# Kernel optimization log

Hardware: AMD Instinct MI355X
Metric: run time of the kernel (lower is better)

## Reference

```python
import jax, jax.numpy as jnp
import numpy as np

B, C, H, W = 4, 256, 64, 64
C8 = C // 8

def setup_inputs() -> dict:
    key = jax.random.key(0)
    ks = jax.random.split(key, 7)
    s = 0.05
    return {
        "x": jax.random.normal(ks[0], (B, C, H, W), dtype=jnp.float32),
        "wq": jax.random.normal(ks[1], (C8, C), dtype=jnp.float32) * s,
        "bq": jax.random.normal(ks[2], (C8,), dtype=jnp.float32) * s,
        "wk": jax.random.normal(ks[3], (C8, C), dtype=jnp.float32) * s,
        "bk": jax.random.normal(ks[4], (C8,), dtype=jnp.float32) * s,
        "wv": jax.random.normal(ks[5], (C, C), dtype=jnp.float32) * s,
        "bv": jax.random.normal(ks[6], (C,), dtype=jnp.float32) * s,
    }

def reference(x, wq, bq, wk, bk, wv, bv):
    b, c, h, w = x.shape
    n = h * w
    xf = x.reshape(b, c, n)                                   # [B,C,N]
    q = jnp.einsum('oc,bcn->bon', wq, xf) + bq[:, None]       # [B,C/8,N]
    k = jnp.einsum('oc,bcn->bon', wk, xf) + bk[:, None]       # [B,C/8,N]
    v = jnp.einsum('oc,bcn->bon', wv, xf) + bv[:, None]       # [B,C,N]
    # attention[b, i, j] = softmax_j( q[b,:,i] . k[b,:,j] )  (no scaling, per original)
    scores = jnp.einsum('bon,bom->bnm', q, k)                 # [B,N,N]
    attn = jax.nn.softmax(scores, axis=-1)
    # out[b,c,i] = sum_j v[b,c,j] * attn[b,i,j]
    out = jnp.einsum('bcm,bnm->bcn', v, attn)                 # [B,C,N]
    return out.reshape(b, c, h, w) + x
```

## Files before the change

### kernel.cpp

```cpp
#include <hip/hip_runtime.h>
#include <cstdint>
#include <cstddef>

#define BB 4
#define CC 256
#define NN 4096
#define CO 32

typedef __attribute__((ext_vector_type(8))) short bf8;
typedef __attribute__((ext_vector_type(4))) float f4;
typedef __attribute__((ext_vector_type(2))) unsigned int u32x2;

#define AS1 __attribute__((address_space(1)))
#define AS3 __attribute__((address_space(3)))

__device__ __forceinline__ unsigned short f2bf(float f) {
    union { float f; unsigned int u; } c; c.f = f;
    unsigned int r = c.u + 0x7FFFu + ((c.u >> 16) & 1u);
    return (unsigned short)(r >> 16);
}
__device__ __forceinline__ float bf2f(unsigned short b) {
    union { unsigned int u; float f; } c; c.u = ((unsigned int)b) << 16;
    return c.f;
}
__device__ __forceinline__ unsigned int cvt_pk_bf16(float a, float b) {
    unsigned int r;
    asm("v_cvt_pk_bf16_f32 %0, %1, %2" : "=v"(r) : "v"(a), "v"(b));
    return r;
}

#define LDS_BARRIER()                                          \
    do {                                                       \
        __builtin_amdgcn_sched_barrier(0);                     \
        asm volatile("s_waitcnt lgkmcnt(0)" ::: "memory");     \
        __builtin_amdgcn_s_barrier();                          \
        __builtin_amdgcn_sched_barrier(0);                     \
    } while (0)

__global__ __launch_bounds__(512, 2) void k_prep(
        const float* __restrict__ x,
        const float* __restrict__ wq, const float* __restrict__ bq,
        const float* __restrict__ wk, const float* __restrict__ bk,
        const float* __restrict__ wv, const float* __restrict__ bv,
        unsigned short* __restrict__ q_hi, unsigned short* __restrict__ q_lo,
        unsigned short* __restrict__ k_hi, unsigned short* __restrict__ k_lo,
        unsigned short* __restrict__ vws) {
    __shared__ float xT[64 * 256];
    int blk = blockIdx.x;
    int it = blk & 63, b = blk >> 6;
    int i0 = it * 64;
    int tid = threadIdx.x, w = tid >> 6, lane = tid & 63;
    int lr = lane & 15, lg = lane >> 4;

    {
        const float* xp = x + (size_t)b * CC * NN + i0;
        int cl = tid >> 4;
        int il = (tid & 15) * 4;
#pragma unroll
        for (int pass = 0; pass < 8; ++pass) {
            int c = pass * 32 + cl;
            f4 v = *(const f4*)(xp + (size_t)c * NN + il);
#pragma unroll
            for (int jj = 0; jj < 4; ++jj) {
                int i = il + jj;
                xT[i * 256 + (((c >> 2) ^ (i & 7)) << 2) + (c & 3)] = v[jj];
            }
        }
    }
    __syncthreads();

    if (w < 4) {
        f4 acc[4] = {};
        for (int ks = 0; ks < 8; ++ks) {
            int i = w * 16 + lr;
            int kc = ks * 32 + lg * 8;
            f4 xa = *(const f4*)&xT[i * 256 + (((kc >> 2) ^ (i & 7)) << 2)];
            f4 xb = *(const f4*)&xT[i * 256 + ((((kc >> 2) + 1) ^ (i & 7)) << 2)];
            bf8 ahi, alo;
#pragma unroll
            for (int e = 0; e < 8; ++e) {
                float f = (e < 4) ? xa[e] : xb[e - 4];
                unsigned short hh = f2bf(f);
                ahi[e] = (short)hh;
                alo[e] = (short)f2bf(f - bf2f(hh));
            }
#pragma unroll
            for (int u = 0; u < 4; ++u) {
                int o = u * 16 + lr;
                const float* wrow = (u < 2) ? (wq + (size_t)o * CC)
                                            : (wk + (size_t)(o - 32) * CC);
                bf8 bhi, blo;
#pragma unroll
                for (int e = 0; e < 8; ++e) {
                    float wvv = wrow[ks * 32 + lg * 8 + e];
                    unsigned short hh = f2bf(wvv);
                    bhi[e] = (short)hh;
                    blo[e] = (short)f2bf(wvv - bf2f(hh));
                }
                acc[u] = __builtin_amdgcn_mfma_f32_16x16x32_bf16(alo, bhi, acc[u], 0, 0, 0);
                acc[u] = __builtin_amdgcn_mfma_f32_16x16x32_bf16(ahi, blo, acc[u], 0, 0, 0);
                acc[u] = __builtin_amdgcn_mfma_f32_16x16x32_bf16(ahi, bhi, acc[u], 0, 0, 0);
            }
        }
#pragma unroll
        for (int u = 0; u < 4; ++u) {
            int o = u * 16 + lr;
            float bias = (u < 2) ? bq[o] : bk[o - 32];
#pragma unroll
            for (int r = 0; r < 4; ++r) {
                int i = i0 + w * 16 + lg * 4 + r;
                float v = acc[u][r] + bias;
                unsigned short hh = f2bf(v);
                unsigned short ll = f2bf(v - bf2f(hh));
                if (u < 2) {
                    size_t off = ((size_t)b * NN + i) * CO + o;
                    q_hi[off] = hh; q_lo[off] = ll;
                } else {
                    size_t off = ((size_t)b * NN + i) * CO + (o - 32);
                    k_hi[off] = hh; k_lo[off] = ll;
                }
            }
        }
    } else {
        int cb = (w - 4) * 64;
        f4 acc[4][4];
#pragma unroll
        for (int u = 0; u < 4; ++u) {
            f4 bias4;
#pragma unroll
            for (int r = 0; r < 4; ++r) bias4[r] = bv[cb + u * 16 + lg * 4 + r];
#pragma unroll
            for (int t = 0; t < 4; ++t) acc[u][t] = bias4;
        }
        for (int ks = 0; ks < 8; ++ks) {
            bf8 bfr[4];
#pragma unroll
            for (int t = 0; t < 4; ++t) {
                int i = t * 16 + lr;
                int kc = ks * 32 + lg * 8;
                f4 xa = *(const f4*)&xT[i * 256 + (((kc >> 2) ^ (i & 7)) << 2)];
                f4 xb = *(const f4*)&xT[i * 256 + ((((kc >> 2) + 1) ^ (i & 7)) << 2)];
#pragma unroll
                for (int e = 0; e < 8; ++e)
                    bfr[t][e] = (short)f2bf((e < 4) ? xa[e] : xb[e - 4]);
            }
#pragma unroll
            for (int u = 0; u < 4; ++u) {
                const float* wrow = wv + (size_t)(cb + u * 16 + lr) * CC + ks * 32 + lg * 8;
                bf8 afr;
#pragma unroll
                for (int e = 0; e < 8; ++e) afr[e] = (short)f2bf(wrow[e]);
#pragma unroll
                for (int t = 0; t < 4; ++t)
                    acc[u][t] = __builtin_amdgcn_mfma_f32_16x16x32_bf16(afr, bfr[t], acc[u][t], 0, 0, 0);
            }
        }
#pragma unroll
        for (int u = 0; u < 4; ++u)
#pragma unroll
            for (int t = 0; t < 4; ++t)
#pragma unroll
                for (int r = 0; r < 4; ++r) {
                    int c = cb + u * 16 + lg * 4 + r;
                    vws[((size_t)b * CC + c) * NN + i0 + t * 16 + lr] = f2bf(acc[u][t][r]);
                }
    }
}

__global__ __launch_bounds__(512, 4) void k_attn(
        const unsigned short* __restrict__ q_hi, const unsigned short* __restrict__ q_lo,
        const unsigned short* __restrict__ k_hi, const unsigned short* __restrict__ k_lo,
        const unsigned short* __restrict__ vws,
        const float* __restrict__ x, float* __restrict__ out) {
    __shared__ unsigned short Vt[2][8192];
    __shared__ unsigned short K2[2][4096];
    __shared__ unsigned short Pt[4096];
    __shared__ float lsum_s[2][64];

    int m = blockIdx.x;
    int xcd = m & 7;
    int b = xcd >> 1;
    int t128 = ((m >> 3) << 1) + (xcd & 1);
    int qblk = t128 >> 1;
    int hc = t128 & 1;
    int i0 = qblk * 64;
    int cb0 = hc * 128;
    int tid = threadIdx.x, w = tid >> 6, lane = tid & 63;
    int lr = lane & 15, lg = lane >> 4;
    int a = w & 3, h = w >> 2;
    int lr7 = lr & 7;

    bf8 qfh, qfl;
    {
        size_t off = ((size_t)b * NN + i0 + a * 16 + lr) * CO + lg * 8;
        qfh = *(const bf8*)(q_hi + off);
        qfl = *(const bf8*)(q_lo + off);
    }

    const unsigned short* vrow  = vws  + (size_t)b * CC * NN;
    const unsigned short* khrow = k_hi + (size_t)b * NN * CO;
    const unsigned short* klrow = k_lo + (size_t)b * NN * CO;

    int l3 = lane >> 3, sl = lane & 7;
    int us = sl ^ l3;
    const unsigned short* vsrc = vrow + (size_t)(cb0 + w * 16 + l3) * NN + us * 8;
    const unsigned short* kbp = (us < 4) ? (khrow + us * 8) : (klrow + (us - 4) * 8);
    const unsigned short* ksrc = kbp + (size_t)(w * 8 + l3) * CO;

    auto stage = [&](int jt, int p) {
        int j0 = jt * 64;
#pragma unroll
        for (int n = 0; n < 2; ++n) {
            __builtin_amdgcn_global_load_lds(
                (const AS1 void*)(vsrc + (size_t)(n * 8) * NN + j0),
                (AS3 void*)(&Vt[p][(w * 16 + n * 8) * 64]), 16, 0, 0);
        }
        __builtin_amdgcn_global_load_lds(
            (const AS1 void*)(ksrc + (size_t)j0 * CO),
            (AS3 void*)(&K2[p][(w * 8) * 64]), 16, 0, 0);
    };

    f4 acc[4] = {};
    float lsum = 0.f;

    stage(0, 0);
    __syncthreads();

    for (int jt = 0; jt < 64; ++jt) {
        int p = jt & 1;
        if (jt < 63) stage(jt + 1, p ^ 1);
#pragma unroll
        for (int jj = 0; jj < 2; ++jj) {
            int jl = h * 32 + jj * 16 + lr;
            bf8 kfh = *(const bf8*)&K2[p][jl * 64 + ((lg ^ lr7)) * 8];
            bf8 kfl = *(const bf8*)&K2[p][jl * 64 + (((4 | lg) ^ lr7)) * 8];
            f4 s = {};
            s = __builtin_amdgcn_mfma_f32_16x16x32_bf16(kfh, qfl, s, 0, 0, 0);
            s = __builtin_amdgcn_mfma_f32_16x16x32_bf16(kfl, qfh, s, 0, 0, 0);
            s = __builtin_amdgcn_mfma_f32_16x16x32_bf16(kfh, qfh, s, 0, 0, 0);
            float e0 = __expf(s[0]), e1 = __expf(s[1]), e2 = __expf(s[2]), e3 = __expf(s[3]);
            lsum += (e0 + e1) + (e2 + e3);
            u32x2 d;
            d[0] = cvt_pk_bf16(e0, e1);
            d[1] = cvt_pk_bf16(e2, e3);
            int slot = (h * 4 + jj * 2 + (lg >> 1)) ^ lr7;
            *(u32x2*)&Pt[(a * 16 + lr) * 64 + slot * 8 + (lg & 1) * 4] = d;
        }
        LDS_BARRIER();
        __builtin_amdgcn_s_setprio(1);
#pragma unroll
        for (int ks = 0; ks < 2; ++ks) {
            bf8 pb[4], vf;
#pragma unroll
            for (int qt = 0; qt < 4; ++qt)
                pb[qt] = *(const bf8*)&Pt[(qt * 16 + lr) * 64 + (((ks * 4 + lg) ^ lr7)) * 8];
            vf = *(const bf8*)&Vt[p][(w * 16 + lr) * 64 + (((ks * 4 + lg) ^ lr7)) * 8];
#pragma unroll
            for (int qt = 0; qt < 4; ++qt)
                acc[qt] = __builtin_amdgcn_mfma_f32_16x16x32_bf16(vf, pb[qt], acc[qt], 0, 0, 0);
        }
        __builtin_amdgcn_s_setprio(0);
        __syncthreads();
    }

    lsum += __shfl_xor(lsum, 16, 64);
    lsum += __shfl_xor(lsum, 32, 64);
    if (lane < 16) lsum_s[h][a * 16 + lane] = lsum;
    __syncthreads();

#pragma unroll
    for (int qt = 0; qt < 4; ++qt) {
        float li = 1.0f / (lsum_s[0][qt * 16 + lr] + lsum_s[1][qt * 16 + lr]);
        int iq = i0 + qt * 16 + lr;
#pragma unroll
        for (int r = 0; r < 4; ++r) {
            int c = cb0 + w * 16 + lg * 4 + r;
            size_t off = ((size_t)(b * CC + c)) * NN + iq;
            out[off] = acc[qt][r] * li + x[off];
        }
    }
}

extern "C" void kernel_launch(void* const* d_in, const int* in_sizes, int n_in,
                              void* d_out, int out_size, void* d_ws, size_t ws_size,
                              hipStream_t stream) {
    const float* x  = (const float*)d_in[0];
    const float* wq = (const float*)d_in[1];
    const float* bq = (const float*)d_in[2];
    const float* wk = (const float*)d_in[3];
    const float* bk = (const float*)d_in[4];
    const float* wv = (const float*)d_in[5];
    const float* bv = (const float*)d_in[6];
    float* out = (float*)d_out;
    char* ws = (char*)d_ws;
    unsigned short* qh = (unsigned short*)(ws);
    unsigned short* ql = (unsigned short*)(ws + 1048576);
    unsigned short* kh = (unsigned short*)(ws + 2097152);
    unsigned short* kl = (unsigned short*)(ws + 3145728);
    unsigned short* vv = (unsigned short*)(ws + 4194304);

    hipLaunchKernelGGL(k_prep, dim3(256), dim3(512), 0, stream,
                       x, wq, bq, wk, bk, wv, bv, qh, ql, kh, kl, vv);
    hipLaunchKernelGGL(k_attn, dim3(512), dim3(512), 0, stream,
                       qh, ql, kh, kl, vv, x, out);
}
```

Baseline: 98.33 us.

## Switch attention to 32x32 MFMA, triple-buffer K and double-buffer P

Rewrites the attention kernel's inner loop to use 32x32x16 bf16 MFMAs for both QK^T and PV. Only half of the waves compute scores. K now uses a 3-stage LDS ring and P a double buffer, so the loop drops to one barrier per iteration with a partial vmcnt wait, letting loads overlap compute. The aim is fewer instructions and less synchronisation per tile. The trade-off is idle waves during the score phase, more LDS use, and new swizzle patterns that have to stay conflict-free and correct.

```diff
diff --git a/kernel.cpp b/kernel.cpp
--- a/kernel.cpp
+++ b/kernel.cpp
@@ -9,6 +9,7 @@
 
 typedef __attribute__((ext_vector_type(8))) short bf8;
 typedef __attribute__((ext_vector_type(4))) float f4;
+typedef __attribute__((ext_vector_type(16))) float f16f;
 typedef __attribute__((ext_vector_type(2))) unsigned int u32x2;
 
 #define AS1 __attribute__((address_space(1)))
@@ -28,14 +29,6 @@
     asm("v_cvt_pk_bf16_f32 %0, %1, %2" : "=v"(r) : "v"(a), "v"(b));
     return r;
 }
-
-#define LDS_BARRIER()                                          \
-    do {                                                       \
-        __builtin_amdgcn_sched_barrier(0);                     \
-        asm volatile("s_waitcnt lgkmcnt(0)" ::: "memory");     \
-        __builtin_amdgcn_s_barrier();                          \
-        __builtin_amdgcn_sched_barrier(0);                     \
-    } while (0)
 
 __global__ __launch_bounds__(512, 2) void k_prep(
         const float* __restrict__ x,
@@ -172,10 +165,10 @@
         const unsigned short* __restrict__ k_hi, const unsigned short* __restrict__ k_lo,
         const unsigned short* __restrict__ vws,
         const float* __restrict__ x, float* __restrict__ out) {
-    __shared__ unsigned short Vt[2][8192];
-    __shared__ unsigned short K2[2][4096];
-    __shared__ unsigned short Pt[4096];
-    __shared__ float lsum_s[2][64];
+    __shared__ __align__(16) unsigned short Vt[2][8192];
+    __shared__ __align__(16) unsigned short K2[3][4096];
+    __shared__ __align__(16) unsigned short P2[2][2][2048];
+    __shared__ float lsum_s[2][2][32];
 
     int m = blockIdx.x;
     int xcd = m & 7;
@@ -186,98 +179,109 @@
     int i0 = qblk * 64;
     int cb0 = hc * 128;
     int tid = threadIdx.x, w = tid >> 6, lane = tid & 63;
-    int lr = lane & 15, lg = lane >> 4;
-    int a = w & 3, h = w >> 2;
-    int lr7 = lr & 7;
-
-    bf8 qfh, qfl;
-    {
-        size_t off = ((size_t)b * NN + i0 + a * 16 + lr) * CO + lg * 8;
-        qfh = *(const bf8*)(q_hi + off);
-        qfl = *(const bf8*)(q_lo + off);
-    }
-
-    const unsigned short* vrow  = vws  + (size_t)b * CC * NN;
-    const unsigned short* khrow = k_hi + (size_t)b * NN * CO;
-    const unsigned short* klrow = k_lo + (size_t)b * NN * CO;
-
+    int l31 = lane & 31, h = lane >> 5;
+    int fsw = (lane & 7) ^ ((lane >> 3) & 3);
+    int jh = w & 1, qh = w >> 1;
+    int cs = w & 3, qhp = w >> 2;
+
+    bf8 qfh[2], qfl[2];
+    if (w < 4) {
+        size_t qoff = ((size_t)b * NN + i0 + qh * 32 + l31) * CO + h * 8;
+        qfh[0] = *(const bf8*)(q_hi + qoff);
+        qfl[0] = *(const bf8*)(q_lo + qoff);
+        qfh[1] = *(const bf8*)(q_hi + qoff + 16);
+        qfl[1] = *(const bf8*)(q_lo + qoff + 16);
+    }
+
+    const unsigned short* vrow = vws + (size_t)b * CC * NN;
     int l3 = lane >> 3, sl = lane & 7;
-    int us = sl ^ l3;
-    const unsigned short* vsrc = vrow + (size_t)(cb0 + w * 16 + l3) * NN + us * 8;
-    const unsigned short* kbp = (us < 4) ? (khrow + us * 8) : (klrow + (us - 4) * 8);
-    const unsigned short* ksrc = kbp + (size_t)(w * 8 + l3) * CO;
-
-    auto stage = [&](int jt, int p) {
-        int j0 = jt * 64;
-#pragma unroll
-        for (int n = 0; n < 2; ++n) {
-            __builtin_amdgcn_global_load_lds(
-                (const AS1 void*)(vsrc + (size_t)(n * 8) * NN + j0),
-                (AS3 void*)(&Vt[p][(w * 16 + n * 8) * 64]), 16, 0, 0);
-        }
-        __builtin_amdgcn_global_load_lds(
-            (const AS1 void*)(ksrc + (size_t)j0 * CO),
+    int usV0 = sl ^ l3 ^ ((2 * w) & 3);
+    int usV1 = usV0 ^ 1;
+    const unsigned short* vsrc0 = vrow + (size_t)(cb0 + w * 16 + l3) * NN + usV0 * 8;
+    const unsigned short* vsrc1 = vrow + (size_t)(cb0 + w * 16 + 8 + l3) * NN + usV1 * 8;
+    int usK = sl ^ l3 ^ (w & 3);
+    const unsigned short* kbase = (usK < 4) ? (k_hi + (size_t)b * NN * CO + usK * 8)
+                                            : (k_lo + (size_t)b * NN * CO + (usK - 4) * 8);
+    const unsigned short* ksrc = kbase + (size_t)(w * 8 + l3) * CO;
+
+    auto stageV = [&](int jt, int p) {
+        int j0 = ((jt < 64) ? jt : 63) * 64;
+        __builtin_amdgcn_global_load_lds((const AS1 void*)(vsrc0 + j0),
+            (AS3 void*)(&Vt[p][(w * 16) * 64]), 16, 0, 0);
+        __builtin_amdgcn_global_load_lds((const AS1 void*)(vsrc1 + j0),
+            (AS3 void*)(&Vt[p][(w * 16 + 8) * 64]), 16, 0, 0);
+    };
+    auto stageK = [&](int jt, int p) {
+        int j0 = ((jt < 64) ? jt : 63) * 64;
+        __builtin_amdgcn_global_load_lds((const AS1 void*)(ksrc + (size_t)j0 * CO),
             (AS3 void*)(&K2[p][(w * 8) * 64]), 16, 0, 0);
     };
 
-    f4 acc[4] = {};
+    f16f acc = {};
     float lsum = 0.f;
 
-    stage(0, 0);
+    stageV(0, 0); stageK(0, 0); stageK(1, 1);
     __syncthreads();
 
     for (int jt = 0; jt < 64; ++jt) {
-        int p = jt & 1;
-        if (jt < 63) stage(jt + 1, p ^ 1);
-#pragma unroll
-        for (int jj = 0; jj < 2; ++jj) {
-            int jl = h * 32 + jj * 16 + lr;
-            bf8 kfh = *(const bf8*)&K2[p][jl * 64 + ((lg ^ lr7)) * 8];
-            bf8 kfl = *(const bf8*)&K2[p][jl * 64 + (((4 | lg) ^ lr7)) * 8];
-            f4 s = {};
-            s = __builtin_amdgcn_mfma_f32_16x16x32_bf16(kfh, qfl, s, 0, 0, 0);
-            s = __builtin_amdgcn_mfma_f32_16x16x32_bf16(kfl, qfh, s, 0, 0, 0);
-            s = __builtin_amdgcn_mfma_f32_16x16x32_bf16(kfh, qfh, s, 0, 0, 0);
-            float e0 = __expf(s[0]), e1 = __expf(s[1]), e2 = __expf(s[2]), e3 = __expf(s[3]);
-            lsum += (e0 + e1) + (e2 + e3);
-            u32x2 d;
-            d[0] = cvt_pk_bf16(e0, e1);
-            d[1] = cvt_pk_bf16(e2, e3);
-            int slot = (h * 4 + jj * 2 + (lg >> 1)) ^ lr7;
-            *(u32x2*)&Pt[(a * 16 + lr) * 64 + slot * 8 + (lg & 1) * 4] = d;
-        }
-        LDS_BARRIER();
+        int pv = jt & 1;
+        int pk = jt % 3;
+        if (w < 4) {
+            const unsigned short* Kp = &K2[pk][(jh * 32 + l31) * 64];
+            f16f s = {};
+#pragma unroll
+            for (int dc = 0; dc < 2; ++dc) {
+                bf8 kfh = *(const bf8*)(Kp + (((2 * dc + h) ^ fsw) * 8));
+                bf8 kfl = *(const bf8*)(Kp + (((4 + 2 * dc + h) ^ fsw) * 8));
+                s = __builtin_amdgcn_mfma_f32_32x32x16_bf16(kfh, qfl[dc], s, 0, 0, 0);
+                s = __builtin_amdgcn_mfma_f32_32x32x16_bf16(kfl, qfh[dc], s, 0, 0, 0);
+                s = __builtin_amdgcn_mfma_f32_32x32x16_bf16(kfh, qfh[dc], s, 0, 0, 0);
+            }
+            unsigned int pk32[8];
+#pragma unroll
+            for (int i = 0; i < 8; ++i) {
+                float e0 = __expf(s[2 * i]), e1 = __expf(s[2 * i + 1]);
+                lsum += e0 + e1;
+                pk32[i] = cvt_pk_bf16(e0, e1);
+            }
+            unsigned short* Pp = &P2[pv][qh][l31 * 64 + h * 4];
+#pragma unroll
+            for (int g = 0; g < 4; ++g) {
+                u32x2 d2; d2[0] = pk32[2 * g]; d2[1] = pk32[2 * g + 1];
+                *(u32x2*)(Pp + (((jh * 4 + g) ^ fsw) * 8)) = d2;
+            }
+        }
+        stageK(jt + 2, (jt + 2) % 3);
+        __builtin_amdgcn_sched_barrier(0);
+        asm volatile("s_waitcnt vmcnt(1) lgkmcnt(0)" ::: "memory");
+        __builtin_amdgcn_s_barrier();
+        __builtin_amdgcn_sched_barrier(0);
         __builtin_amdgcn_s_setprio(1);
-#pragma unroll
-        for (int ks = 0; ks < 2; ++ks) {
-            bf8 pb[4], vf;
-#pragma unroll
-            for (int qt = 0; qt < 4; ++qt)
-                pb[qt] = *(const bf8*)&Pt[(qt * 16 + lr) * 64 + (((ks * 4 + lg) ^ lr7)) * 8];
-            vf = *(const bf8*)&Vt[p][(w * 16 + lr) * 64 + (((ks * 4 + lg) ^ lr7)) * 8];
-#pragma unroll
-            for (int qt = 0; qt < 4; ++qt)
-                acc[qt] = __builtin_amdgcn_mfma_f32_16x16x32_bf16(vf, pb[qt], acc[qt], 0, 0, 0);
+        {
+            const unsigned short* Pr = &P2[pv][qhp][l31 * 64];
+            const unsigned short* Vr = &Vt[pv][(cs * 32 + l31) * 64];
+#pragma unroll
+            for (int kc = 0; kc < 4; ++kc) {
+                bf8 pb = *(const bf8*)(Pr + (((2 * kc + h) ^ fsw) * 8));
+                bf8 vf = *(const bf8*)(Vr + (((2 * kc + h) ^ fsw) * 8));
+                acc = __builtin_amdgcn_mfma_f32_32x32x16_bf16(vf, pb, acc, 0, 0, 0);
+            }
         }
         __builtin_amdgcn_s_setprio(0);
-        __syncthreads();
-    }
-
-    lsum += __shfl_xor(lsum, 16, 64);
+        stageV(jt + 1, pv ^ 1);
+    }
+
     lsum += __shfl_xor(lsum, 32, 64);
-    if (lane < 16) lsum_s[h][a * 16 + lane] = lsum;
+    if (w < 4 && lane < 32) lsum_s[qh][jh][l31] = lsum;
     __syncthreads();
 
-#pragma unroll
-    for (int qt = 0; qt < 4; ++qt) {
-        float li = 1.0f / (lsum_s[0][qt * 16 + lr] + lsum_s[1][qt * 16 + lr]);
-        int iq = i0 + qt * 16 + lr;
-#pragma unroll
-        for (int r = 0; r < 4; ++r) {
-            int c = cb0 + w * 16 + lg * 4 + r;
-            size_t off = ((size_t)(b * CC + c)) * NN + iq;
-            out[off] = acc[qt][r] * li + x[off];
-        }
+    float linv = 1.0f / (lsum_s[qhp][0][l31] + lsum_s[qhp][1][l31]);
+    int iq = i0 + qhp * 32 + l31;
+#pragma unroll
+    for (int r = 0; r < 16; ++r) {
+        int c = cb0 + cs * 32 + (r & 3) + 8 * (r >> 2) + 4 * h;
+        size_t off = ((size_t)(b * CC + c)) * NN + iq;
+        out[off] = acc[r] * linv + x[off];
     }
 }
 
```

Result: slower. 103.1 us (+4.9%).

## Load V directly to registers and switch PV to 32x32x16 MFMA

Applied to the files above, without the earlier changes.

The P·V stage now uses 32x32x16 bf16 MFMAs, with each wave owning a 32-channel by 32-query tile. V fragments are loaded straight from global memory into double-buffered registers one tile ahead, so the V staging buffer in LDS is removed. A manual vmcnt wait plus barrier replaces __syncthreads, and the P tile uses a new row-dependent swizzle. The aim is to cut LDS traffic and footprint and to issue fewer, larger MFMAs. In exchange it adds register pressure and relies on global load latency being hidden within one iteration.

```diff
diff --git a/kernel.cpp b/kernel.cpp
--- a/kernel.cpp
+++ b/kernel.cpp
@@ -9,6 +9,7 @@
 
 typedef __attribute__((ext_vector_type(8))) short bf8;
 typedef __attribute__((ext_vector_type(4))) float f4;
+typedef __attribute__((ext_vector_type(16))) float f16f;
 typedef __attribute__((ext_vector_type(2))) unsigned int u32x2;
 
 #define AS1 __attribute__((address_space(1)))
@@ -172,9 +173,8 @@
         const unsigned short* __restrict__ k_hi, const unsigned short* __restrict__ k_lo,
         const unsigned short* __restrict__ vws,
         const float* __restrict__ x, float* __restrict__ out) {
-    __shared__ unsigned short Vt[2][8192];
-    __shared__ unsigned short K2[2][4096];
-    __shared__ unsigned short Pt[4096];
+    __shared__ __align__(16) unsigned short K2[2][4096];
+    __shared__ __align__(16) unsigned short Pt[4096];
     __shared__ float lsum_s[2][64];
 
     int m = blockIdx.x;
@@ -186,9 +186,10 @@
     int i0 = qblk * 64;
     int cb0 = hc * 128;
     int tid = threadIdx.x, w = tid >> 6, lane = tid & 63;
-    int lr = lane & 15, lg = lane >> 4;
+    int lr = lane & 15, lg = lane >> 4, lr7 = lr & 7;
     int a = w & 3, h = w >> 2;
-    int lr7 = lr & 7;
+    int l31 = lane & 31, hh = lane >> 5;
+    int cs = w & 3, qhp = w >> 2;
 
     bf8 qfh, qfl;
     {
@@ -197,43 +198,37 @@
         qfl = *(const bf8*)(q_lo + off);
     }
 
-    const unsigned short* vrow  = vws  + (size_t)b * CC * NN;
-    const unsigned short* khrow = k_hi + (size_t)b * NN * CO;
-    const unsigned short* klrow = k_lo + (size_t)b * NN * CO;
-
     int l3 = lane >> 3, sl = lane & 7;
-    int us = sl ^ l3;
-    const unsigned short* vsrc = vrow + (size_t)(cb0 + w * 16 + l3) * NN + us * 8;
-    const unsigned short* kbp = (us < 4) ? (khrow + us * 8) : (klrow + (us - 4) * 8);
-    const unsigned short* ksrc = kbp + (size_t)(w * 8 + l3) * CO;
-
-    auto stage = [&](int jt, int p) {
-        int j0 = jt * 64;
-#pragma unroll
-        for (int n = 0; n < 2; ++n) {
-            __builtin_amdgcn_global_load_lds(
-                (const AS1 void*)(vsrc + (size_t)(n * 8) * NN + j0),
-                (AS3 void*)(&Vt[p][(w * 16 + n * 8) * 64]), 16, 0, 0);
-        }
-        __builtin_amdgcn_global_load_lds(
-            (const AS1 void*)(ksrc + (size_t)j0 * CO),
+    int usK = sl ^ l3;
+    const unsigned short* kbase = (usK < 4) ? (k_hi + (size_t)b * NN * CO + usK * 8)
+                                            : (k_lo + (size_t)b * NN * CO + (usK - 4) * 8);
+    const unsigned short* ksrc = kbase + (size_t)(w * 8 + l3) * CO;
+    auto stageK = [&](int jt, int p) {
+        int j0 = ((jt < 64) ? jt : 63) * 64;
+        __builtin_amdgcn_global_load_lds((const AS1 void*)(ksrc + (size_t)j0 * CO),
             (AS3 void*)(&K2[p][(w * 8) * 64]), 16, 0, 0);
     };
 
-    f4 acc[4] = {};
+    const unsigned short* vsrcb = vws + ((size_t)b * CC + cb0 + cs * 32 + l31) * NN + hh * 8;
+
+    f16f acc = {};
     float lsum = 0.f;
-
-    stage(0, 0);
+    bf8 vA[4], vB[4];
+
+    stageK(0, 0);
+#pragma unroll
+    for (int kc = 0; kc < 4; ++kc) vA[kc] = *(const bf8*)(vsrcb + kc * 16);
     __syncthreads();
 
-    for (int jt = 0; jt < 64; ++jt) {
+    auto iter = [&](int jt, bf8 (&vc)[4], bf8 (&vn)[4]) {
         int p = jt & 1;
-        if (jt < 63) stage(jt + 1, p ^ 1);
-#pragma unroll
-        for (int jj = 0; jj < 2; ++jj) {
-            int jl = h * 32 + jj * 16 + lr;
-            bf8 kfh = *(const bf8*)&K2[p][jl * 64 + ((lg ^ lr7)) * 8];
-            bf8 kfl = *(const bf8*)&K2[p][jl * 64 + (((4 | lg) ^ lr7)) * 8];
+        stageK(jt + 1, p ^ 1);
+#pragma unroll
+        for (int t = 0; t < 2; ++t) {
+            int jl = h * 32 + t * 16 + lr;
+            const unsigned short* Kp = &K2[p][jl * 64];
+            bf8 kfh = *(const bf8*)(Kp + ((lg ^ lr7)) * 8);
+            bf8 kfl = *(const bf8*)(Kp + (((4 | lg) ^ lr7)) * 8);
             f4 s = {};
             s = __builtin_amdgcn_mfma_f32_16x16x32_bf16(kfh, qfl, s, 0, 0, 0);
             s = __builtin_amdgcn_mfma_f32_16x16x32_bf16(kfl, qfh, s, 0, 0, 0);
@@ -243,24 +238,39 @@
             u32x2 d;
             d[0] = cvt_pk_bf16(e0, e1);
             d[1] = cvt_pk_bf16(e2, e3);
-            int slot = (h * 4 + jj * 2 + (lg >> 1)) ^ lr7;
-            *(u32x2*)&Pt[(a * 16 + lr) * 64 + slot * 8 + (lg & 1) * 4] = d;
+            int row = a * 16 + lr;
+            int swz = (row ^ (row >> 3)) & 7;
+            int slot = (h * 4 + t * 2 + (lg >> 1)) ^ swz;
+            *(u32x2*)&Pt[row * 64 + slot * 8 + (lg & 1) * 4] = d;
         }
         LDS_BARRIER();
         __builtin_amdgcn_s_setprio(1);
-#pragma unroll
-        for (int ks = 0; ks < 2; ++ks) {
-            bf8 pb[4], vf;
-#pragma unroll
-            for (int qt = 0; qt < 4; ++qt)
-                pb[qt] = *(const bf8*)&Pt[(qt * 16 + lr) * 64 + (((ks * 4 + lg) ^ lr7)) * 8];
-            vf = *(const bf8*)&Vt[p][(w * 16 + lr) * 64 + (((ks * 4 + lg) ^ lr7)) * 8];
-#pragma unroll
-            for (int qt = 0; qt < 4; ++qt)
-                acc[qt] = __builtin_amdgcn_mfma_f32_16x16x32_bf16(vf, pb[qt], acc[qt], 0, 0, 0);
+        {
+            int prow = qhp * 32 + l31;
+            int pswz = (prow ^ (prow >> 3)) & 7;
+            const unsigned short* Pr = &Pt[prow * 64];
+#pragma unroll
+            for (int kc = 0; kc < 4; ++kc) {
+                bf8 pb = *(const bf8*)(Pr + (((kc * 2 + hh) ^ pswz)) * 8);
+                acc = __builtin_amdgcn_mfma_f32_32x32x16_bf16(vc[kc], pb, acc, 0, 0, 0);
+            }
         }
         __builtin_amdgcn_s_setprio(0);
-        __syncthreads();
+        {
+            int j0n = ((jt + 1 < 64) ? (jt + 1) : 63) * 64;
+#pragma unroll
+            for (int kc = 0; kc < 4; ++kc)
+                vn[kc] = *(const bf8*)(vsrcb + j0n + kc * 16);
+        }
+        __builtin_amdgcn_sched_barrier(0);
+        asm volatile("s_waitcnt vmcnt(4) lgkmcnt(0)" ::: "memory");
+        __builtin_amdgcn_s_barrier();
+        __builtin_amdgcn_sched_barrier(0);
+    };
+
+    for (int jt = 0; jt < 64; jt += 2) {
+        iter(jt, vA, vB);
+        iter(jt + 1, vB, vA);
     }
 
     lsum += __shfl_xor(lsum, 16, 64);
@@ -268,16 +278,13 @@
     if (lane < 16) lsum_s[h][a * 16 + lane] = lsum;
     __syncthreads();
 
-#pragma unroll
-    for (int qt = 0; qt < 4; ++qt) {
-        float li = 1.0f / (lsum_s[0][qt * 16 + lr] + lsum_s[1][qt * 16 + lr]);
-        int iq = i0 + qt * 16 + lr;
-#pragma unroll
-        for (int r = 0; r < 4; ++r) {
-            int c = cb0 + w * 16 + lg * 4 + r;
-            size_t off = ((size_t)(b * CC + c)) * NN + iq;
-            out[off] = acc[qt][r] * li + x[off];
-        }
+    float linv = 1.0f / (lsum_s[0][qhp * 32 + l31] + lsum_s[1][qhp * 32 + l31]);
+    int iq = i0 + qhp * 32 + l31;
+#pragma unroll
+    for (int r = 0; r < 16; ++r) {
+        int c = cb0 + cs * 32 + (r & 3) + 8 * (r >> 2) + 4 * hh;
+        size_t off = ((size_t)(b * CC + c)) * NN + iq;
+        out[off] = acc[r] * linv + x[off];
     }
 }
 
```

Result: slower. 155.3 us (+57.9%).
